# Kernel optimization log

Hardware: AMD Instinct MI355X
Metric: run time of the kernel (lower is better)

## Reference

```python
import jax, jax.numpy as jnp
import numpy as np

N_NODES = 50000
N_EDGES = 800000
IN_FEATS = 64
HIDDEN = 64
NUM_CLASSES = 32


def _graph_conv(x, src, dst, W, b, n_nodes):
    # DGL GraphConv, norm='both', allow_zero_in_degree=True:
    # out = D_in^{-1/2} * (A^T @ (D_out^{-1/2} * x)) @ W + b, degrees clamped to >=1
    e = src.shape[0]
    ones = jnp.ones((e,), dtype=x.dtype)
    out_deg = jax.ops.segment_sum(ones, src, num_segments=n_nodes)
    in_deg = jax.ops.segment_sum(ones, dst, num_segments=n_nodes)
    norm_src = jax.lax.rsqrt(jnp.maximum(out_deg, 1.0))[:, None]
    norm_dst = jax.lax.rsqrt(jnp.maximum(in_deg, 1.0))[:, None]
    h = x * norm_src                                   # [N, d]
    agg = jax.ops.segment_sum(h[src], dst, num_segments=n_nodes)  # gather+scatter over edges
    return (agg * norm_dst) @ W + b


def setup_inputs() -> dict:
    key = jax.random.key(0)
    k1, k2, k3, k4, k5 = jax.random.split(key, 5)
    features = jax.random.normal(k1, (N_NODES, IN_FEATS), dtype=jnp.float32)
    src = jax.random.randint(k2, (N_EDGES,), 0, N_NODES, dtype=jnp.int32)
    dst = jax.random.randint(k3, (N_EDGES,), 0, N_NODES, dtype=jnp.int32)
    W1 = jax.random.normal(k4, (IN_FEATS, HIDDEN), dtype=jnp.float32) * (1.0 / np.sqrt(IN_FEATS))
    b1 = jnp.zeros((HIDDEN,), dtype=jnp.float32)
    W2 = jax.random.normal(k5, (HIDDEN, NUM_CLASSES), dtype=jnp.float32) * (1.0 / np.sqrt(HIDDEN))
    b2 = jnp.zeros((NUM_CLASSES,), dtype=jnp.float32)
    return {"features": features, "src": src, "dst": dst,
            "W1": W1, "b1": b1, "W2": W2, "b2": b2}


def reference(features, src, dst, W1, b1, W2, b2) -> jnp.ndarray:
    n = features.shape[0]
    h = jax.nn.relu(_graph_conv(features, src, dst, W1, b1, n))
    out = _graph_conv(h, src, dst, W2, b2, n)
    # single canonical etype -> mean over one-element stack is identity
    return out
```

## Files before the change

kernel.cpp:

```cpp
#include <hip/hip_runtime.h>
#include <hip/hip_bf16.h>

#define N_NODES 50000
#define N_EDGES 800000
#define F 64
#define C 32
#define CAP 48

#define NPB   200
#define EPB   4000
#define NBUCK 196

__global__ void part_count_kernel(const int* __restrict__ src, const int* __restrict__ dst,
                                  int* __restrict__ bcnt_d, int* __restrict__ bcnt_s) {
    __shared__ int hd[NBUCK], hs[NBUCK];
    int t = threadIdx.x;
    for (int i = t; i < NBUCK; i += 256) { hd[i] = 0; hs[i] = 0; }
    __syncthreads();
    int b0 = blockIdx.x * EPB;
    for (int i = b0 + t; i < b0 + EPB; i += 256) {
        atomicAdd(&hd[dst[i] >> 8], 1);
        atomicAdd(&hs[src[i] >> 8], 1);
    }
    __syncthreads();
    for (int i = t; i < NBUCK; i += 256) {
        bcnt_d[blockIdx.x * NBUCK + i] = hd[i];
        bcnt_s[blockIdx.x * NBUCK + i] = hs[i];
    }
}

__global__ void part_scan_kernel(const int* __restrict__ bcnt_d, const int* __restrict__ bcnt_s,
                                 int* __restrict__ eoff_d, int* __restrict__ eoff_s,
                                 int* __restrict__ base_d, int* __restrict__ base_s) {
    __shared__ int tot_d[NBUCK], tot_s[NBUCK], bd[NBUCK + 1], bs[NBUCK + 1];
    int t = threadIdx.x;
    if (t < NBUCK) {
        int run = 0;
        for (int blk = 0; blk < NPB; blk++) {
            eoff_d[blk * NBUCK + t] = run;
            run += bcnt_d[blk * NBUCK + t];
        }
        tot_d[t] = run;
        run = 0;
        for (int blk = 0; blk < NPB; blk++) {
            eoff_s[blk * NBUCK + t] = run;
            run += bcnt_s[blk * NBUCK + t];
        }
        tot_s[t] = run;
    }
    __syncthreads();
    if (t == 0) {
        int r = 0;
        for (int b = 0; b < NBUCK; b++) { bd[b] = r; r += tot_d[b]; }
        bd[NBUCK] = r;
        r = 0;
        for (int b = 0; b < NBUCK; b++) { bs[b] = r; r += tot_s[b]; }
        bs[NBUCK] = r;
    }
    __syncthreads();
    if (t < NBUCK + 1) { base_d[t] = bd[t]; base_s[t] = bs[t]; }
}

__global__ void part_scatter_kernel(const int* __restrict__ src, const int* __restrict__ dst,
                                    const int* __restrict__ eoff_d, const int* __restrict__ eoff_s,
                                    const int* __restrict__ base_d, const int* __restrict__ base_s,
                                    int* __restrict__ edge_d, int* __restrict__ edge_s) {
    __shared__ int cd[NBUCK], cs[NBUCK];
    int t = threadIdx.x;
    for (int i = t; i < NBUCK; i += 256) {
        cd[i] = base_d[i] + eoff_d[blockIdx.x * NBUCK + i];
        cs[i] = base_s[i] + eoff_s[blockIdx.x * NBUCK + i];
    }
    __syncthreads();
    int b0 = blockIdx.x * EPB;
    for (int i = b0 + t; i < b0 + EPB; i += 256) {
        int d = dst[i], s = src[i];
        int p = atomicAdd(&cd[d >> 8], 1);
        edge_d[p] = ((d & 255) << 16) | s;
        int q = atomicAdd(&cs[s >> 8], 1);
        edge_s[q] = s & 255;
    }
}

__global__ void bucket_build_kernel(const int* __restrict__ edge_d, const int* __restrict__ edge_s,
                                    const int* __restrict__ base_d, const int* __restrict__ base_s,
                                    int* __restrict__ csr, int* __restrict__ cnt,
                                    float* __restrict__ norm_dst, float* __restrict__ norm_src) {
    __shared__ int cur[256];
    __shared__ int hs[256];
    int t = threadIdx.x;
    int bucket = blockIdx.x;
    cur[t] = 0;
    hs[t] = 0;
    __syncthreads();
    int lo = base_d[bucket], hi = base_d[bucket + 1];
    for (int i = lo + t; i < hi; i += 256) {
        int pd = edge_d[i];
        int dlow = pd >> 16;
        int s = pd & 0xFFFF;
        int pos = atomicAdd(&cur[dlow], 1);
        if (pos < CAP) csr[(size_t)(bucket * 256 + dlow) * CAP + pos] = s;
    }
    int slo = base_s[bucket], shi = base_s[bucket + 1];
    for (int i = slo + t; i < shi; i += 256) {
        atomicAdd(&hs[edge_s[i]], 1);
    }
    __syncthreads();
    int node = bucket * 256 + t;
    if (node < N_NODES) {
        int c = cur[t] < CAP ? cur[t] : CAP;
        cnt[node] = c;
        norm_dst[node] = rsqrtf(fmaxf((float)c, 1.0f));
        norm_src[node] = rsqrtf(fmaxf((float)hs[t], 1.0f));
    }
}

__global__ void gemm_y_kernel(const float* __restrict__ x,
                              const float* __restrict__ ns,
                              const float* __restrict__ W,
                              __hip_bfloat16* __restrict__ y) {
    __shared__ float sW[F * F];
    __shared__ float srow[16][F];
    int t = threadIdx.x;
    for (int i = t; i < F * F; i += 256) sW[i] = W[i];
    int j = t & 63;
    int w = t >> 6;
    int base = blockIdx.x * 16;
    for (int r = w; r < 16; r += 4) srow[r][j] = x[(size_t)(base + r) * F + j];
    __syncthreads();
    float a0 = 0, a1 = 0, a2 = 0, a3 = 0;
#pragma unroll
    for (int k = 0; k < F; k++) {
        float wv = sW[k * F + j];
        a0 += srow[w * 4 + 0][k] * wv;
        a1 += srow[w * 4 + 1][k] * wv;
        a2 += srow[w * 4 + 2][k] * wv;
        a3 += srow[w * 4 + 3][k] * wv;
    }
    int n0 = base + w * 4;
    y[(size_t)(n0 + 0) * F + j] = __float2bfloat16(a0 * ns[n0 + 0]);
    y[(size_t)(n0 + 1) * F + j] = __float2bfloat16(a1 * ns[n0 + 1]);
    y[(size_t)(n0 + 2) * F + j] = __float2bfloat16(a2 * ns[n0 + 2]);
    y[(size_t)(n0 + 3) * F + j] = __float2bfloat16(a3 * ns[n0 + 3]);
}

__global__ void gather64_kernel(const __hip_bfloat16* __restrict__ y,
                                const int* __restrict__ csr,
                                const int* __restrict__ cnt,
                                const float* __restrict__ norm_dst,
                                const float* __restrict__ norm_src,
                                const float* __restrict__ b1,
                                __hip_bfloat16* __restrict__ h2) {
    int gid  = blockIdx.x * blockDim.x + threadIdx.x;
    int node = gid >> 6;
    int lane = threadIdx.x & 63;
    if (node >= N_NODES) return;
    int n = cnt[node];
    const int* row = csr + (size_t)node * CAP;
    float acc = 0.0f;
    int e = 0;
    for (; e + 3 < n; e += 4) {
        int sa = row[e], sb = row[e + 1], sc = row[e + 2], sd = row[e + 3];
        acc += __bfloat162float(y[(size_t)sa * F + lane]);
        acc += __bfloat162float(y[(size_t)sb * F + lane]);
        acc += __bfloat162float(y[(size_t)sc * F + lane]);
        acc += __bfloat162float(y[(size_t)sd * F + lane]);
    }
    for (; e < n; e++) acc += __bfloat162float(y[(size_t)row[e] * F + lane]);
    float v = fmaxf(acc * norm_dst[node] + b1[lane], 0.0f);
    h2[(size_t)node * F + lane] = __float2bfloat16(v * norm_src[node]);
}

__global__ void gather_gemm2_kernel(const __hip_bfloat16* __restrict__ h2,
                                    const int* __restrict__ csr,
                                    const int* __restrict__ cnt,
                                    const float* __restrict__ norm_dst,
                                    const float* __restrict__ W2,
                                    const float* __restrict__ b2,
                                    float* __restrict__ out) {
    __shared__ float sW[F * C];
    __shared__ float sagg[4][F];
    int t = threadIdx.x;
    for (int i = t; i < F * C; i += 256) sW[i] = W2[i];
    int w    = t >> 6;
    int lane = t & 63;
    int node = blockIdx.x * 4 + w;
    float acc = 0.0f;
    if (node < N_NODES) {
        int n = cnt[node];
        const int* row = csr + (size_t)node * CAP;
        int e = 0;
        for (; e + 3 < n; e += 4) {
            int sa = row[e], sb = row[e + 1], sc = row[e + 2], sd = row[e + 3];
            acc += __bfloat162float(h2[(size_t)sa * F + lane]);
            acc += __bfloat162float(h2[(size_t)sb * F + lane]);
            acc += __bfloat162float(h2[(size_t)sc * F + lane]);
            acc += __bfloat162float(h2[(size_t)sd * F + lane]);
        }
        for (; e < n; e++) acc += __bfloat162float(h2[(size_t)row[e] * F + lane]);
    }
    sagg[w][lane] = acc;
    __syncthreads();
    int j    = lane & 31;
    int half = lane >> 5;
    float o = 0.0f;
    if (node < N_NODES) {
#pragma unroll
        for (int k = 0; k < 32; k++) {
            int kk = half * 32 + k;
            o += sagg[w][kk] * sW[kk * C + j];
        }
    }
    o += __shfl_down(o, 32);
    if (node < N_NODES && half == 0)
        out[(size_t)node * C + j] = o * norm_dst[node] + b2[j];
}

extern "C" void kernel_launch(void* const* d_in, const int* in_sizes, int n_in,
                              void* d_out, int out_size, void* d_ws, size_t ws_size,
                              hipStream_t stream) {
    const float* features = (const float*)d_in[0];
    const int*   src      = (const int*)d_in[1];
    const int*   dst      = (const int*)d_in[2];
    const float* W1       = (const float*)d_in[3];
    const float* b1       = (const float*)d_in[4];
    const float* W2       = (const float*)d_in[5];
    const float* b2       = (const float*)d_in[6];
    float* out = (float*)d_out;

    char* p = (char*)d_ws;
    float* norm_src = (float*)p;  p += (size_t)N_NODES * 4;
    float* norm_dst = (float*)p;  p += (size_t)N_NODES * 4;
    int*   cnt      = (int*)p;    p += (size_t)N_NODES * 4;
    int*   csr      = (int*)p;    p += (size_t)N_NODES * CAP * 4;
    __hip_bfloat16* y  = (__hip_bfloat16*)p;  p += (size_t)N_NODES * F * 2;
    __hip_bfloat16* h2 = (__hip_bfloat16*)p;

    int* edge_d = (int*)y;
    int* edge_s = edge_d + N_EDGES;
    int* q = (int*)h2;
    int* bcnt_d = q;                 q += NPB * NBUCK;
    int* bcnt_s = q;                 q += NPB * NBUCK;
    int* eoff_d = q;                 q += NPB * NBUCK;
    int* eoff_s = q;                 q += NPB * NBUCK;
    int* base_d = q;                 q += NBUCK + 1;
    int* base_s = q;

    part_count_kernel<<<NPB, 256, 0, stream>>>(src, dst, bcnt_d, bcnt_s);
    part_scan_kernel<<<1, 256, 0, stream>>>(bcnt_d, bcnt_s, eoff_d, eoff_s, base_d, base_s);
    part_scatter_kernel<<<NPB, 256, 0, stream>>>(src, dst, eoff_d, eoff_s, base_d, base_s,
                                                 edge_d, edge_s);
    bucket_build_kernel<<<NBUCK, 256, 0, stream>>>(edge_d, edge_s, base_d, base_s,
                                                   csr, cnt, norm_dst, norm_src);

    gemm_y_kernel<<<N_NODES / 16, 256, 0, stream>>>(features, norm_src, W1, y);
    gather64_kernel<<<(N_NODES * 64) / 256, 256, 0, stream>>>(y, csr, cnt, norm_dst,
                                                              norm_src, b1, h2);

    gather_gemm2_kernel<<<(N_NODES + 3) / 4, 256, 0, stream>>>(h2, csr, cnt, norm_dst,
                                                               W2, b2, out);
}
```

Measured before the change: 226.7 us.

## Split layer-1 gather into feature halves and apply W2 before layer-2 gather

Layer-1 features are stored as two 32-wide bf16 tables, each gathered in its own pass, so each pass has a smaller working set that fits cache better. Each pass splits the edges between two half-waves and combines them with a shuffle. Layer 2 now multiplies by W2 first in a separate GEMM, so the second gather reads 32-wide bf16 rows instead of 64-wide, halving its gather traffic. The cost is extra kernel launches and reading the CSR index rows twice in layer 1.

```diff
diff --git a/kernel.cpp b/kernel.cpp
--- a/kernel.cpp
+++ b/kernel.cpp
@@ -118,7 +118,8 @@
 __global__ void gemm_y_kernel(const float* __restrict__ x,
                               const float* __restrict__ ns,
                               const float* __restrict__ W,
-                              __hip_bfloat16* __restrict__ y) {
+                              __hip_bfloat16* __restrict__ yA,
+                              __hip_bfloat16* __restrict__ yB) {
     __shared__ float sW[F * F];
     __shared__ float srow[16][F];
     int t = threadIdx.x;
@@ -138,82 +139,88 @@
         a3 += srow[w * 4 + 3][k] * wv;
     }
     int n0 = base + w * 4;
-    y[(size_t)(n0 + 0) * F + j] = __float2bfloat16(a0 * ns[n0 + 0]);
-    y[(size_t)(n0 + 1) * F + j] = __float2bfloat16(a1 * ns[n0 + 1]);
-    y[(size_t)(n0 + 2) * F + j] = __float2bfloat16(a2 * ns[n0 + 2]);
-    y[(size_t)(n0 + 3) * F + j] = __float2bfloat16(a3 * ns[n0 + 3]);
-}
-
-__global__ void gather64_kernel(const __hip_bfloat16* __restrict__ y,
-                                const int* __restrict__ csr,
-                                const int* __restrict__ cnt,
-                                const float* __restrict__ norm_dst,
-                                const float* __restrict__ norm_src,
-                                const float* __restrict__ b1,
-                                __hip_bfloat16* __restrict__ h2) {
+    __hip_bfloat16* half = (j < 32) ? yA : yB;
+    int jj = j & 31;
+    half[(size_t)(n0 + 0) * 32 + jj] = __float2bfloat16(a0 * ns[n0 + 0]);
+    half[(size_t)(n0 + 1) * 32 + jj] = __float2bfloat16(a1 * ns[n0 + 1]);
+    half[(size_t)(n0 + 2) * 32 + jj] = __float2bfloat16(a2 * ns[n0 + 2]);
+    half[(size_t)(n0 + 3) * 32 + jj] = __float2bfloat16(a3 * ns[n0 + 3]);
+}
+
+__global__ void gather_half_kernel(const __hip_bfloat16* __restrict__ ytab,
+                                   const int* __restrict__ csr,
+                                   const int* __restrict__ cnt,
+                                   const float* __restrict__ norm_dst,
+                                   const float* __restrict__ norm_src,
+                                   const float* __restrict__ b1,
+                                   int off,
+                                   __hip_bfloat16* __restrict__ h2) {
     int gid  = blockIdx.x * blockDim.x + threadIdx.x;
     int node = gid >> 6;
+    if (node >= N_NODES) return;
     int lane = threadIdx.x & 63;
-    if (node >= N_NODES) return;
+    int feat = lane & 31;
+    int half = lane >> 5;
     int n = cnt[node];
     const int* row = csr + (size_t)node * CAP;
     float acc = 0.0f;
-    int e = 0;
-    for (; e + 3 < n; e += 4) {
-        int sa = row[e], sb = row[e + 1], sc = row[e + 2], sd = row[e + 3];
-        acc += __bfloat162float(y[(size_t)sa * F + lane]);
-        acc += __bfloat162float(y[(size_t)sb * F + lane]);
-        acc += __bfloat162float(y[(size_t)sc * F + lane]);
-        acc += __bfloat162float(y[(size_t)sd * F + lane]);
-    }
-    for (; e < n; e++) acc += __bfloat162float(y[(size_t)row[e] * F + lane]);
-    float v = fmaxf(acc * norm_dst[node] + b1[lane], 0.0f);
-    h2[(size_t)node * F + lane] = __float2bfloat16(v * norm_src[node]);
-}
-
-__global__ void gather_gemm2_kernel(const __hip_bfloat16* __restrict__ h2,
-                                    const int* __restrict__ csr,
-                                    const int* __restrict__ cnt,
-                                    const float* __restrict__ norm_dst,
-                                    const float* __restrict__ W2,
-                                    const float* __restrict__ b2,
-                                    float* __restrict__ out) {
+    int e = half;
+    for (; e + 2 < n; e += 4) {
+        int s0 = row[e], s1 = row[e + 2];
+        acc += __bfloat162float(ytab[(size_t)s0 * 32 + feat]);
+        acc += __bfloat162float(ytab[(size_t)s1 * 32 + feat]);
+    }
+    for (; e < n; e += 2) acc += __bfloat162float(ytab[(size_t)row[e] * 32 + feat]);
+    acc += __shfl_down(acc, 32);
+    if (half == 0) {
+        float v = fmaxf(acc * norm_dst[node] + b1[off + feat], 0.0f);
+        h2[(size_t)node * F + off + feat] = __float2bfloat16(v * norm_src[node]);
+    }
+}
+
+__global__ void gemm_g_kernel(const __hip_bfloat16* __restrict__ h2,
+                              const float* __restrict__ W,
+                              __hip_bfloat16* __restrict__ g) {
     __shared__ float sW[F * C];
-    __shared__ float sagg[4][F];
-    int t = threadIdx.x;
-    for (int i = t; i < F * C; i += 256) sW[i] = W2[i];
-    int w    = t >> 6;
-    int lane = t & 63;
-    int node = blockIdx.x * 4 + w;
+    __shared__ float srow[8][F];
+    int t = threadIdx.x;
+    for (int i = t; i < F * C; i += 256) sW[i] = W[i];
+    int local = t >> 5;
+    int j     = t & 31;
+    int node  = blockIdx.x * 8 + local;
+    srow[local][j]      = __bfloat162float(h2[(size_t)node * F + j]);
+    srow[local][j + 32] = __bfloat162float(h2[(size_t)node * F + j + 32]);
+    __syncthreads();
     float acc = 0.0f;
-    if (node < N_NODES) {
-        int n = cnt[node];
-        const int* row = csr + (size_t)node * CAP;
-        int e = 0;
-        for (; e + 3 < n; e += 4) {
-            int sa = row[e], sb = row[e + 1], sc = row[e + 2], sd = row[e + 3];
-            acc += __bfloat162float(h2[(size_t)sa * F + lane]);
-            acc += __bfloat162float(h2[(size_t)sb * F + lane]);
-            acc += __bfloat162float(h2[(size_t)sc * F + lane]);
-            acc += __bfloat162float(h2[(size_t)sd * F + lane]);
-        }
-        for (; e < n; e++) acc += __bfloat162float(h2[(size_t)row[e] * F + lane]);
-    }
-    sagg[w][lane] = acc;
-    __syncthreads();
-    int j    = lane & 31;
+#pragma unroll
+    for (int k = 0; k < F; k++) acc += srow[local][k] * sW[k * C + j];
+    g[(size_t)node * C + j] = __float2bfloat16(acc);
+}
+
+__global__ void gather_out_kernel(const __hip_bfloat16* __restrict__ g,
+                                  const int* __restrict__ csr,
+                                  const int* __restrict__ cnt,
+                                  const float* __restrict__ norm_dst,
+                                  const float* __restrict__ b2,
+                                  float* __restrict__ out) {
+    int gid  = blockIdx.x * blockDim.x + threadIdx.x;
+    int node = gid >> 6;
+    if (node >= N_NODES) return;
+    int lane = threadIdx.x & 63;
+    int feat = lane & 31;
     int half = lane >> 5;
-    float o = 0.0f;
-    if (node < N_NODES) {
-#pragma unroll
-        for (int k = 0; k < 32; k++) {
-            int kk = half * 32 + k;
-            o += sagg[w][kk] * sW[kk * C + j];
-        }
-    }
-    o += __shfl_down(o, 32);
-    if (node < N_NODES && half == 0)
-        out[(size_t)node * C + j] = o * norm_dst[node] + b2[j];
+    int n = cnt[node];
+    const int* row = csr + (size_t)node * CAP;
+    float acc = 0.0f;
+    int e = half;
+    for (; e + 2 < n; e += 4) {
+        int s0 = row[e], s1 = row[e + 2];
+        acc += __bfloat162float(g[(size_t)s0 * C + feat]);
+        acc += __bfloat162float(g[(size_t)s1 * C + feat]);
+    }
+    for (; e < n; e += 2) acc += __bfloat162float(g[(size_t)row[e] * C + feat]);
+    acc += __shfl_down(acc, 32);
+    if (half == 0) out[(size_t)node * C + feat] = acc * norm_dst[node] + b2[feat];
 }
 
 extern "C" void kernel_launch(void* const* d_in, const int* in_sizes, int n_in,
@@ -233,10 +240,12 @@
     float* norm_dst = (float*)p;  p += (size_t)N_NODES * 4;
     int*   cnt      = (int*)p;    p += (size_t)N_NODES * 4;
     int*   csr      = (int*)p;    p += (size_t)N_NODES * CAP * 4;
-    __hip_bfloat16* y  = (__hip_bfloat16*)p;  p += (size_t)N_NODES * F * 2;
+    __hip_bfloat16* yA = (__hip_bfloat16*)p;  p += (size_t)N_NODES * 32 * 2;
+    __hip_bfloat16* yB = (__hip_bfloat16*)p;  p += (size_t)N_NODES * 32 * 2;
     __hip_bfloat16* h2 = (__hip_bfloat16*)p;
-
-    int* edge_d = (int*)y;
+    __hip_bfloat16* g  = yA;
+
+    int* edge_d = (int*)yA;
     int* edge_s = edge_d + N_EDGES;
     int* q = (int*)h2;
     int* bcnt_d = q;                 q += NPB * NBUCK;
@@ -253,10 +262,13 @@
     bucket_build_kernel<<<NBUCK, 256, 0, stream>>>(edge_d, edge_s, base_d, base_s,
                                                    csr, cnt, norm_dst, norm_src);
 
-    gemm_y_kernel<<<N_NODES / 16, 256, 0, stream>>>(features, norm_src, W1, y);
-    gather64_kernel<<<(N_NODES * 64) / 256, 256, 0, stream>>>(y, csr, cnt, norm_dst,
-                                                              norm_src, b1, h2);
-
-    gather_gemm2_kernel<<<(N_NODES + 3) / 4, 256, 0, stream>>>(h2, csr, cnt, norm_dst,
-                                                               W2, b2, out);
-}
+    gemm_y_kernel<<<N_NODES / 16, 256, 0, stream>>>(features, norm_src, W1, yA, yB);
+    gather_half_kernel<<<(N_NODES * 64) / 256, 256, 0, stream>>>(yA, csr, cnt, norm_dst,
+                                                                 norm_src, b1, 0, h2);
+    gather_half_kernel<<<(N_NODES * 64) / 256, 256, 0, stream>>>(yB, csr, cnt, norm_dst,
+                                                                 norm_src, b1, 32, h2);
+
+    gemm_g_kernel<<<N_NODES / 8, 256, 0, stream>>>(h2, W2, g);
+    gather_out_kernel<<<(N_NODES * 64) / 256, 256, 0, stream>>>(g, csr, cnt, norm_dst,
+                                                                b2, out);
+}
```

After: 240.4 us. 1.06x slower.
